# Kernel tuning notes

Measured on AMD Instinct MI355X. Metric: run time of the kernel, lower is better.

Reference implementation:

```python
import jax, jax.numpy as jnp
import numpy as np

DIM = 1024
N_HEAD = 16
N_KV_HEAD = 4
HEAD_DIM = DIM // N_HEAD  # 64
INTER = 2688
B, N = 2, 2048
EPS = 1e-6


def setup_inputs() -> dict:
    key = jax.random.key(0)
    ks = jax.random.split(key, 10)
    std = 0.02
    x = jax.random.normal(ks[0], (B, N, DIM), dtype=jnp.float32)
    # rotary embedding: theta = pos * 10000^(-2i/d), cos/sin of shape [N, HEAD_DIM//2]
    inv_freq = 1.0 / (10000.0 ** (np.arange(0, HEAD_DIM, 2, dtype=np.float32) / HEAD_DIM))
    t = np.arange(N, dtype=np.float32)
    ang = np.outer(t, inv_freq)  # [N, HEAD_DIM//2]
    rope_cos = jnp.asarray(np.cos(ang))
    rope_sin = jnp.asarray(np.sin(ang))
    mask = jnp.tril(jnp.ones((N, N), dtype=bool))  # True = attend
    return {
        "x": x,
        "w_attn_norm": jnp.ones((DIM,), jnp.float32),
        "w_ffn_norm": jnp.ones((DIM,), jnp.float32),
        "Wq": jax.random.normal(ks[1], (DIM, N_HEAD * HEAD_DIM), jnp.float32) * std,
        "Wkv": jax.random.normal(ks[2], (DIM, 2 * N_KV_HEAD * HEAD_DIM), jnp.float32) * std,
        "Wo": jax.random.normal(ks[3], (N_HEAD * HEAD_DIM, DIM), jnp.float32) * std,
        "W1": jax.random.normal(ks[4], (DIM, INTER), jnp.float32) * std,
        "W2": jax.random.normal(ks[5], (INTER, DIM), jnp.float32) * std,
        "W3": jax.random.normal(ks[6], (DIM, INTER), jnp.float32) * std,
        "rope_cos": rope_cos,
        "rope_sin": rope_sin,
        "mask": mask,
    }


def _rms_norm(x, w):
    # nn.functional.rms_norm: x / sqrt(mean(x^2) + eps) * w
    return x * jax.lax.rsqrt(jnp.mean(x * x, axis=-1, keepdims=True) + EPS) * w


def _apply_rope(x, cos, sin):
    # x: [b, n, h, d]; consecutive pairs (x[2k], x[2k+1]) form complex numbers
    xr = x[..., 0::2]
    xi = x[..., 1::2]
    c = cos[None, :, None, :]
    s = sin[None, :, None, :]
    yr = xr * c - xi * s
    yi = xr * s + xi * c
    return jnp.stack([yr, yi], axis=-1).reshape(x.shape)


def _block(x, w_attn_norm, w_ffn_norm, Wq, Wkv, Wo, W1, W2, W3, rope_cos, rope_sin, mask):
    b, n, _ = x.shape
    # --- attention (GQA, use_cache=False prefill) ---
    h = _rms_norm(x, w_attn_norm)
    q = (h @ Wq).reshape(b, n, N_HEAD, HEAD_DIM)
    kv = h @ Wkv
    k, v = jnp.split(kv, 2, axis=-1)
    k = k.reshape(b, n, N_KV_HEAD, HEAD_DIM)
    v = v.reshape(b, n, N_KV_HEAD, HEAD_DIM)
    q = _apply_rope(q, rope_cos, rope_sin)
    k = _apply_rope(k, rope_cos, rope_sin)
    # einops repeat 'b n h d -> b n (r h) d' == tile along head axis
    r = N_HEAD // N_KV_HEAD
    k = jnp.tile(k, (1, 1, r, 1))
    v = jnp.tile(v, (1, 1, r, 1))
    scale = HEAD_DIM ** -0.5
    scores = jnp.einsum('bnhd,bmhd->bhnm', q, k) * scale
    scores = jnp.where(mask[None, None, :, :], scores, jnp.finfo(scores.dtype).min)
    attn = jax.nn.softmax(scores, axis=-1)
    o = jnp.einsum('bhnm,bmhd->bnhd', attn, v).reshape(b, n, N_HEAD * HEAD_DIM)
    x = x + o @ Wo
    # --- SwiGLU MLP ---
    h2 = _rms_norm(x, w_ffn_norm)
    ff = (jax.nn.silu(h2 @ W1) * (h2 @ W3)) @ W2
    return x + ff


def reference(x, w_attn_norm, w_ffn_norm, Wq, Wkv, Wo, W1, W2, W3, rope_cos, rope_sin, mask):
    return _block(x, w_attn_norm, w_ffn_norm, Wq, Wkv, Wo, W1, W2, W3, rope_cos, rope_sin, mask)
```

## Files before the change

### kernel.cpp

```cpp
#include <hip/hip_runtime.h>

#define DIM 1024
#define NH 16
#define NKV 4
#define HD 64
#define INTER 2688
#define BB 2
#define NN 2048
#define MM (BB*NN)

typedef __attribute__((ext_vector_type(4))) float f32x4;
typedef __attribute__((ext_vector_type(16))) float f32x16;
typedef __attribute__((ext_vector_type(8))) short short8;

#define CROW(r,h) ((((r)&3)) + 8*((r)>>2) + 4*(h))

__device__ __forceinline__ unsigned short f2bf(float f) {
  union { float f; unsigned u; } v; v.f = f;
  unsigned r = v.u + 0x7fffu + ((v.u >> 16) & 1u);
  return (unsigned short)(r >> 16);
}

__device__ __forceinline__ void glds16(const unsigned short* g, unsigned short* l) {
  __builtin_amdgcn_global_load_lds(
      (const __attribute__((address_space(1))) void*)g,
      (__attribute__((address_space(3))) void*)l, 16, 0, 0);
}

__device__ __forceinline__ void xcd_map(int& bx, int& by) {
  int gx = gridDim.x;
  int nwg = gx * gridDim.y;
  int bid = (int)blockIdx.y * gx + (int)blockIdx.x;
  int cpx = nwg >> 3;
  int lg = (bid & 7) * cpx + (bid >> 3);
  bx = lg % gx;
  by = lg / gx;
}

__global__ void transpose_all(const float* __restrict__ Wq, const float* __restrict__ Wkv,
                              const float* __restrict__ Wo, const float* __restrict__ W1,
                              const float* __restrict__ W3, const float* __restrict__ W2,
                              unsigned short* __restrict__ WqkvT, unsigned short* __restrict__ WoT,
                              unsigned short* __restrict__ W1T, unsigned short* __restrict__ W3T,
                              unsigned short* __restrict__ W2T) {
  int tb = blockIdx.x;
  const float* src; unsigned short* dst; int K, Nc, t0;
  if (tb < 1024)        { src = Wq;  dst = WqkvT;                         K = 1024; Nc = 1024; t0 = tb; }
  else if (tb < 1536)   { src = Wkv; dst = WqkvT + (size_t)1024 * 1024;   K = 1024; Nc = 512;  t0 = tb - 1024; }
  else if (tb < 2560)   { src = Wo;  dst = WoT;                           K = 1024; Nc = 1024; t0 = tb - 1536; }
  else if (tb < 5248)   { src = W1;  dst = W1T;                           K = 1024; Nc = 2688; t0 = tb - 2560; }
  else if (tb < 7936)   { src = W3;  dst = W3T;                           K = 1024; Nc = 2688; t0 = tb - 5248; }
  else                  { src = W2;  dst = W2T;                           K = 2688; Nc = 1024; t0 = tb - 7936; }
  int ntx = Nc >> 5;
  int n0 = (t0 % ntx) * 32, k0 = (t0 / ntx) * 32;
  __shared__ float tile[32][33];
  int tx = threadIdx.x & 31, ty = threadIdx.x >> 5;
#pragma unroll
  for (int i = 0; i < 32; i += 8)
    tile[ty + i][tx] = src[(size_t)(k0 + ty + i) * Nc + n0 + tx];
  __syncthreads();
#pragma unroll
  for (int i = 0; i < 32; i += 8)
    dst[(size_t)(n0 + ty + i) * K + k0 + tx] = f2bf(tile[tx][ty + i]);
}

__global__ void rmsnorm_k(const float* __restrict__ x, const float* __restrict__ w,
                          unsigned short* __restrict__ h) {
  int row = blockIdx.x;
  int t = threadIdx.x;
  const float4* xr = (const float4*)(x + (size_t)row * DIM);
  float4 v = xr[t];
  float ss = v.x * v.x + v.y * v.y + v.z * v.z + v.w * v.w;
#pragma unroll
  for (int o = 1; o < 64; o <<= 1) ss += __shfl_xor(ss, o);
  __shared__ float ps[4];
  if ((t & 63) == 0) ps[t >> 6] = ss;
  __syncthreads();
  float r = rsqrtf((ps[0] + ps[1] + ps[2] + ps[3]) * (1.0f / DIM) + 1e-6f);
  const float4* wr = (const float4*)w;
  float4 wv = wr[t];
  ushort4 o4;
  o4.x = f2bf(v.x * r * wv.x);
  o4.y = f2bf(v.y * r * wv.y);
  o4.z = f2bf(v.z * r * wv.z);
  o4.w = f2bf(v.w * r * wv.w);
  *(ushort4*)(h + (size_t)row * DIM + t * 4) = o4;
}

template <bool RES>
__global__ __launch_bounds__(256, 3) void gemm_f32(
    const unsigned short* __restrict__ A, const unsigned short* __restrict__ Bt,
    const float* __restrict__ res, float* __restrict__ C, int Nc, int K) {
  __shared__ __align__(16) unsigned short Asm[3][128 * 32];
  __shared__ __align__(16) unsigned short Bsm[3][128 * 32];
  int tid = threadIdx.x;
  int w = tid >> 6, l = tid & 63;
  int bx, by;
  xcd_map(bx, by);
  int bm = by * 128, bn = bx * 128;
  int wr = (w >> 1) * 64, wc = (w & 1) * 64;
  int c0 = l & 15, g = l >> 4;

  int sr = w * 32 + (l >> 2);
  int sc = ((l & 3) ^ ((sr >> 1) & 3)) * 8;
  const unsigned short* gA0 = A + (size_t)(bm + sr) * K + sc;
  const unsigned short* gA1 = A + (size_t)(bm + sr + 16) * K + sc;
  const unsigned short* gB0 = Bt + (size_t)(bn + sr) * K + sc;
  const unsigned short* gB1 = Bt + (size_t)(bn + sr + 16) * K + sc;
  int ls0 = (w * 32) * 32, ls1 = (w * 32 + 16) * 32;

  int aoff[4], boff[4];
#pragma unroll
  for (int m = 0; m < 4; m++) {
    int ra = wr + m * 16 + c0;
    aoff[m] = ra * 32 + (g ^ ((ra >> 1) & 3)) * 8;
    int rb = wc + m * 16 + c0;
    boff[m] = rb * 32 + (g ^ ((rb >> 1) & 3)) * 8;
  }

  f32x4 acc[4][4] = {};
  int T = K / 32;
  glds16(gA0, &Asm[0][ls0]);
  glds16(gA1, &Asm[0][ls1]);
  glds16(gB0, &Bsm[0][ls0]);
  glds16(gB1, &Bsm[0][ls1]);
  glds16(gA0 + 32, &Asm[1][ls0]);
  glds16(gA1 + 32, &Asm[1][ls1]);
  glds16(gB0 + 32, &Bsm[1][ls0]);
  glds16(gB1 + 32, &Bsm[1][ls1]);
  int cur = 0;
  for (int t = 0; t < T; ++t) {
    if (t + 2 < T) {
      int nx = cur + 2; if (nx >= 3) nx -= 3;
      int ko = (t + 2) * 32;
      glds16(gA0 + ko, &Asm[nx][ls0]);
      glds16(gA1 + ko, &Asm[nx][ls1]);
      glds16(gB0 + ko, &Bsm[nx][ls0]);
      glds16(gB1 + ko, &Bsm[nx][ls1]);
      asm volatile("s_waitcnt vmcnt(8)" ::: "memory");
    } else if (t + 2 == T) {
      asm volatile("s_waitcnt vmcnt(4)" ::: "memory");
    } else {
      asm volatile("s_waitcnt vmcnt(0)" ::: "memory");
    }
    __builtin_amdgcn_s_barrier();
    __builtin_amdgcn_sched_barrier(0);
    const unsigned short* As = Asm[cur];
    const unsigned short* Bs = Bsm[cur];
    short8 af[4], bf[4];
#pragma unroll
    for (int m = 0; m < 4; m++) af[m] = *(const short8*)&As[aoff[m]];
#pragma unroll
    for (int n = 0; n < 4; n++) bf[n] = *(const short8*)&Bs[boff[n]];
    __builtin_amdgcn_s_setprio(1);
#pragma unroll
    for (int m = 0; m < 4; m++)
#pragma unroll
      for (int n = 0; n < 4; n++)
        acc[m][n] = __builtin_amdgcn_mfma_f32_16x16x32_bf16(af[m], bf[n], acc[m][n], 0, 0, 0);
    __builtin_amdgcn_s_setprio(0);
    asm volatile("s_waitcnt lgkmcnt(0)" ::: "memory");
    __builtin_amdgcn_sched_barrier(0);
    __builtin_amdgcn_s_barrier();
    cur = cur + 1 == 3 ? 0 : cur + 1;
  }
  int gq = l >> 4;
#pragma unroll
  for (int m = 0; m < 4; m++) {
#pragma unroll
    for (int i = 0; i < 4; i++) {
      int row = bm + wr + m * 16 + gq * 4 + i;
#pragma unroll
      for (int n = 0; n < 4; n++) {
        int col = bn + wc + n * 16 + c0;
        float v = acc[m][n][i];
        if (RES) v += res[(size_t)row * Nc + col];
        C[(size_t)row * Nc + col] = v;
      }
    }
  }
}

__global__ __launch_bounds__(256, 2) void gemm_ffn13(
    const unsigned short* __restrict__ A, const unsigned short* __restrict__ B1t,
    const unsigned short* __restrict__ B3t, unsigned short* __restrict__ G,
    int Nc, int K) {
  __shared__ __align__(16) unsigned short Asm[2][128 * 32];
  __shared__ __align__(16) unsigned short B1sm[2][128 * 32];
  __shared__ __align__(16) unsigned short B3sm[2][128 * 32];
  int tid = threadIdx.x;
  int w = tid >> 6, l = tid & 63;
  int bx, by;
  xcd_map(bx, by);
  int bm = by * 128, bn = bx * 128;
  int wr = (w >> 1) * 64, wc = (w & 1) * 64;
  int c0 = l & 15, g = l >> 4;

  int sr = w * 32 + (l >> 2);
  int sc = ((l & 3) ^ ((sr >> 1) & 3)) * 8;
  const unsigned short* gA0 = A + (size_t)(bm + sr) * K + sc;
  const unsigned short* gA1 = A + (size_t)(bm + sr + 16) * K + sc;
  const unsigned short* gB1a = B1t + (size_t)(bn + sr) * K + sc;
  const unsigned short* gB1b = B1t + (size_t)(bn + sr + 16) * K + sc;
  const unsigned short* gB3a = B3t + (size_t)(bn + sr) * K + sc;
  const unsigned short* gB3b = B3t + (size_t)(bn + sr + 16) * K + sc;
  int ls0 = (w * 32) * 32, ls1 = (w * 32 + 16) * 32;

  int aoff[4], boff[4];
#pragma unroll
  for (int m = 0; m < 4; m++) {
    int ra = wr + m * 16 + c0;
    aoff[m] = ra * 32 + (g ^ ((ra >> 1) & 3)) * 8;
    int rb = wc + m * 16 + c0;
    boff[m] = rb * 32 + (g ^ ((rb >> 1) & 3)) * 8;
  }

  f32x4 a1[4][4] = {};
  f32x4 a3[4][4] = {};
  int T = K / 32;
  glds16(gA0, &Asm[0][ls0]);
  glds16(gA1, &Asm[0][ls1]);
  glds16(gB1a, &B1sm[0][ls0]);
  glds16(gB1b, &B1sm[0][ls1]);
  glds16(gB3a, &B3sm[0][ls0]);
  glds16(gB3b, &B3sm[0][ls1]);
  __syncthreads();
  int buf = 0;
  for (int t = 0; t < T; ++t) {
    int nb = buf ^ 1;
    if (t + 1 < T) {
      int ko = (t + 1) * 32;
      glds16(gA0 + ko, &Asm[nb][ls0]);
      glds16(gA1 + ko, &Asm[nb][ls1]);
      glds16(gB1a + ko, &B1sm[nb][ls0]);
      glds16(gB1b + ko, &B1sm[nb][ls1]);
      glds16(gB3a + ko, &B3sm[nb][ls0]);
      glds16(gB3b + ko, &B3sm[nb][ls1]);
    }
    const unsigned short* As = Asm[buf];
    const unsigned short* B1s = B1sm[buf];
    const unsigned short* B3s = B3sm[buf];
    short8 af[4], b1f[4], b3f[4];
#pragma unroll
    for (int m = 0; m < 4; m++) af[m] = *(const short8*)&As[aoff[m]];
#pragma unroll
    for (int n = 0; n < 4; n++) {
      b1f[n] = *(const short8*)&B1s[boff[n]];
      b3f[n] = *(const short8*)&B3s[boff[n]];
    }
    __builtin_amdgcn_s_setprio(1);
#pragma unroll
    for (int m = 0; m < 4; m++)
#pragma unroll
      for (int n = 0; n < 4; n++) {
        a1[m][n] = __builtin_amdgcn_mfma_f32_16x16x32_bf16(af[m], b1f[n], a1[m][n], 0, 0, 0);
        a3[m][n] = __builtin_amdgcn_mfma_f32_16x16x32_bf16(af[m], b3f[n], a3[m][n], 0, 0, 0);
      }
    __builtin_amdgcn_s_setprio(0);
    __syncthreads();
    buf = nb;
  }
  int gq = l >> 4;
#pragma unroll
  for (int m = 0; m < 4; m++) {
#pragma unroll
    for (int i = 0; i < 4; i++) {
      int row = bm + wr + m * 16 + gq * 4 + i;
#pragma unroll
      for (int n = 0; n < 4; n++) {
        int col = bn + wc + n * 16 + c0;
        float x1 = a1[m][n][i], x3 = a3[m][n][i];
        float sg = x1 / (1.0f + __expf(-x1));
        G[(size_t)row * Nc + col] = f2bf(sg * x3);
      }
    }
  }
}

__global__ void prep_qkv(const float* __restrict__ qkv, const float* __restrict__ cosb,
                         const float* __restrict__ sinb, unsigned short* __restrict__ qb,
                         unsigned short* __restrict__ kb, unsigned short* __restrict__ vtb) {
  const float QS = 0.125f * 1.44269504f;
  int n = blockIdx.x, b = blockIdx.y;
  int t = threadIdx.x;
  const float* row = qkv + ((size_t)b * NN + n) * 1536;
#pragma unroll
  for (int p = t; p < 512; p += 256) {
    int head = p >> 5, j = p & 31;
    float xr = row[head * 64 + 2 * j], xi = row[head * 64 + 2 * j + 1];
    float c = cosb[n * 32 + j], s = sinb[n * 32 + j];
    size_t o = (((size_t)(b * NH + head)) * NN + n) * 64 + 2 * j;
    qb[o] = f2bf((xr * c - xi * s) * QS);
    qb[o + 1] = f2bf((xr * s + xi * c) * QS);
  }
  if (t < 128) {
    int kvh = t >> 5, j = t & 31;
    float xr = row[1024 + kvh * 64 + 2 * j], xi = row[1024 + kvh * 64 + 2 * j + 1];
    float c = cosb[n * 32 + j], s = sinb[n * 32 + j];
    size_t o = (((size_t)(b * NKV + kvh)) * NN + n) * 64 + 2 * j;
    kb[o] = f2bf(xr * c - xi * s);
    kb[o + 1] = f2bf(xr * s + xi * c);
  }
  {
    int kvh = t >> 6, d = t & 63;
    float v = row[1280 + kvh * 64 + d];
    vtb[(((size_t)(b * NKV + kvh)) * 64 + d) * NN + n] = f2bf(v);
  }
}

__global__ __launch_bounds__(256, 3) void attn_k(
    const unsigned short* __restrict__ qg_, const unsigned short* __restrict__ kg_,
    const unsigned short* __restrict__ vg_, unsigned short* __restrict__ ob) {
  __shared__ __align__(16) unsigned short Ksm[2][64 * 64];
  __shared__ __align__(16) unsigned short Vsm[2][64 * 64];
  int qb = (blockIdx.z == 0) ? (int)blockIdx.x : ((int)gridDim.x - 1 - (int)blockIdx.x);
  int h = blockIdx.y, b = blockIdx.z;
  int kvh = h & 3;
  int tid = threadIdx.x, w = tid >> 6, l = tid & 63;
  int q5 = l & 31, hi = l >> 5;
  int qwbase = qb * 128 + w * 32;
  int qgl = qwbase + q5;

  const unsigned short* Kg = kg_ + ((size_t)(b * NKV + kvh)) * NN * 64;
  const unsigned short* Vg = vg_ + ((size_t)(b * NKV + kvh)) * 64 * NN;

  short8 qf[4];
  {
    const unsigned short* qrow = qg_ + (((size_t)(b * NH + h)) * NN + qgl) * 64 + hi * 8;
#pragma unroll
    for (int d = 0; d < 4; d++) qf[d] = *(const short8*)(qrow + d * 16);
  }

  int srow = l >> 3;
  int schunk = (l & 7) ^ (srow & 7);
  const unsigned short* gK = Kg + (size_t)(w * 16 + srow) * 64 + schunk * 8;
  const unsigned short* gV = Vg + (size_t)(w * 16 + srow) * NN + schunk * 8;

  int nkt = qb * 2 + 2;
  int nkt_w = ((qwbase + 31) >> 6) + 1;

  f32x16 O0 = {}, O1 = {};
  float m_r = -1e30f, l_r = 0.0f;

  glds16(gK, &Ksm[0][w * 1024]);
  glds16(gK + 8 * 64, &Ksm[0][w * 1024 + 512]);
  glds16(gV, &Vsm[0][w * 1024]);
  glds16(gV + 8 * NN, &Vsm[0][w * 1024 + 512]);
  __syncthreads();

  int buf = 0;
  for (int kt = 0; kt < nkt; ++kt) {
    int n0 = kt * 64;
    if (kt + 1 < nkt) {
      int nb = buf ^ 1;
      glds16(gK + (size_t)(n0 + 64) * 64, &Ksm[nb][w * 1024]);
      glds16(gK + (size_t)(n0 + 64) * 64 + 8 * 64, &Ksm[nb][w * 1024 + 512]);
      glds16(gV + n0 + 64, &Vsm[nb][w * 1024]);
      glds16(gV + 8 * NN + n0 + 64, &Vsm[nb][w * 1024 + 512]);
    }
    if (kt < nkt_w) {
      const unsigned short* Ks = Ksm[buf];
      const unsigned short* Vs = Vsm[buf];
      f32x16 S[2];
      __builtin_amdgcn_s_setprio(1);
#pragma unroll
      for (int s = 0; s < 2; s++) {
        f32x16 acc = {};
        int row = s * 32 + q5;
#pragma unroll
        for (int d = 0; d < 4; d++) {
          int ch = (2 * d + hi) ^ (row & 7);
          short8 kf = *(const short8*)&Ks[row * 64 + ch * 8];
          acc = __builtin_amdgcn_mfma_f32_32x32x16_bf16(kf, qf[d], acc, 0, 0, 0);
        }
        S[s] = acc;
      }
      __builtin_amdgcn_s_setprio(0);
      if (kt == nkt_w - 1) {
#pragma unroll
        for (int s = 0; s < 2; s++)
#pragma unroll
          for (int r = 0; r < 16; r++) {
            int kg = n0 + s * 32 + CROW(r, hi);
            S[s][r] = (kg > qgl) ? -1e30f : S[s][r];
          }
      }
      float t16[16];
#pragma unroll
      for (int r = 0; r < 16; r++) t16[r] = fmaxf(S[0][r], S[1][r]);
#pragma unroll
      for (int k = 8; k >= 1; k >>= 1)
#pragma unroll
        for (int r = 0; r < k; r++) t16[r] = fmaxf(t16[r], t16[r + k]);
      float pm = fmaxf(t16[0], __shfl_xor(t16[0], 32));
      if (!__all(pm <= m_r + 8.0f)) {
        float mn = fmaxf(m_r, pm);
        float alpha = exp2f(m_r - mn);
        m_r = mn;
        l_r *= alpha;
        float ab[16];
#pragma unroll
        for (int r = 0; r < 16; r++) ab[r] = __shfl(alpha, CROW(r, 0) + 4 * hi);
#pragma unroll
        for (int r = 0; r < 16; r++) { O0[r] *= ab[r]; O1[r] *= ab[r]; }
      }
#pragma unroll
      for (int s = 0; s < 2; s++)
#pragma unroll
        for (int r = 0; r < 16; r++) S[s][r] = exp2f(S[s][r] - m_r);
      float u[16];
#pragma unroll
      for (int r = 0; r < 16; r++) u[r] = S[0][r] + S[1][r];
#pragma unroll
      for (int k = 8; k >= 1; k >>= 1)
#pragma unroll
        for (int r = 0; r < k; r++) u[r] += u[r + k];
      l_r += (u[0] + __shfl_xor(u[0], 32));
      short8 paf[4];
#pragma unroll
      for (int ks = 0; ks < 4; ks++) {
        const int s = ks >> 1, e = ks & 1;
        unsigned a0, a1, b0, b1;
        asm("v_cvt_pk_bf16_f32 %0, %1, %2" : "=v"(a0) : "v"(S[s][8*e+0]), "v"(S[s][8*e+1]));
        asm("v_cvt_pk_bf16_f32 %0, %1, %2" : "=v"(a1) : "v"(S[s][8*e+2]), "v"(S[s][8*e+3]));
        asm("v_cvt_pk_bf16_f32 %0, %1, %2" : "=v"(b0) : "v"(S[s][8*e+4]), "v"(S[s][8*e+5]));
        asm("v_cvt_pk_bf16_f32 %0, %1, %2" : "=v"(b1) : "v"(S[s][8*e+6]), "v"(S[s][8*e+7]));
        asm("v_permlane32_swap_b32 %0, %1" : "+v"(a0), "+v"(b0));
        asm("v_permlane32_swap_b32 %0, %1" : "+v"(a1), "+v"(b1));
        union { unsigned u4[4]; short8 s8; } pk;
        pk.u4[0] = a0; pk.u4[1] = a1; pk.u4[2] = b0; pk.u4[3] = b1;
        paf[ks] = pk.s8;
      }
      __builtin_amdgcn_s_setprio(1);
#pragma unroll
      for (int ks = 0; ks < 4; ks++) {
        int row0 = q5, row1 = 32 + q5;
        short8 vf0 = *(const short8*)&Vs[row0 * 64 + (((2 * ks + hi) ^ (row0 & 7)) * 8)];
        short8 vf1 = *(const short8*)&Vs[row1 * 64 + (((2 * ks + hi) ^ (row1 & 7)) * 8)];
        O0 = __builtin_amdgcn_mfma_f32_32x32x16_bf16(paf[ks], vf0, O0, 0, 0, 0);
        O1 = __builtin_amdgcn_mfma_f32_32x32x16_bf16(paf[ks], vf1, O1, 0, 0, 0);
      }
      __builtin_amdgcn_s_setprio(0);
    }
    __syncthreads();
    buf ^= 1;
  }
  float linv = 1.0f / l_r;
  float lb[16];
#pragma unroll
  for (int r = 0; r < 16; r++) lb[r] = __shfl(linv, CROW(r, 0) + 4 * hi);
#pragma unroll
  for (int r = 0; r < 16; r++) {
    int orow = qwbase + CROW(r, hi);
    size_t base = ((size_t)b * NN + orow) * 1024 + h * 64 + q5;
    ob[base] = f2bf(O0[r] * lb[r]);
    ob[base + 32] = f2bf(O1[r] * lb[r]);
  }
}

extern "C" void kernel_launch(void* const* d_in, const int* in_sizes, int n_in,
                              void* d_out, int out_size, void* d_ws, size_t ws_size,
                              hipStream_t stream) {
  (void)in_sizes; (void)n_in; (void)out_size; (void)ws_size;
  const float* x    = (const float*)d_in[0];
  const float* w_an = (const float*)d_in[1];
  const float* w_fn = (const float*)d_in[2];
  const float* Wq   = (const float*)d_in[3];
  const float* Wkv  = (const float*)d_in[4];
  const float* Wo   = (const float*)d_in[5];
  const float* W1   = (const float*)d_in[6];
  const float* W2   = (const float*)d_in[7];
  const float* W3   = (const float*)d_in[8];
  const float* cosb = (const float*)d_in[9];
  const float* sinb = (const float*)d_in[10];
  float* out = (float*)d_out;

  char* ws = (char*)d_ws;
  size_t off = 0;
  auto take = [&](size_t bytes) {
    size_t r = off;
    off += (bytes + 255) & ~(size_t)255;
    return r;
  };
  unsigned short* WqkvT = (unsigned short*)(ws + take((size_t)1536 * 1024 * 2));
  unsigned short* WoT   = (unsigned short*)(ws + take((size_t)1024 * 1024 * 2));
  unsigned short* W1T   = (unsigned short*)(ws + take((size_t)2688 * 1024 * 2));
  unsigned short* W3T   = (unsigned short*)(ws + take((size_t)2688 * 1024 * 2));
  unsigned short* W2T   = (unsigned short*)(ws + take((size_t)2688 * 1024 * 2));
  unsigned short* hA    = (unsigned short*)(ws + take((size_t)MM * DIM * 2));
  char* qkv_region = ws + take((size_t)MM * 1536 * 4);
  float* qkv = (float*)qkv_region;
  unsigned short* gbuf = (unsigned short*)qkv_region;
  unsigned short* qbuf = (unsigned short*)(ws + take((size_t)MM * DIM * 2));
  unsigned short* kbuf = (unsigned short*)(ws + take((size_t)BB * NKV * NN * HD * 2));
  unsigned short* vtb  = (unsigned short*)(ws + take((size_t)BB * NKV * NN * HD * 2));
  unsigned short* obuf = (unsigned short*)(ws + take((size_t)MM * DIM * 2));
  float* x2 = (float*)(ws + take((size_t)MM * DIM * 4));

  transpose_all<<<10624, 256, 0, stream>>>(Wq, Wkv, Wo, W1, W3, W2,
                                           WqkvT, WoT, W1T, W3T, W2T);
  rmsnorm_k<<<MM, 256, 0, stream>>>(x, w_an, hA);
  gemm_f32<false><<<dim3(1536 / 128, MM / 128), 256, 0, stream>>>(hA, WqkvT, nullptr, qkv, 1536, 1024);
  prep_qkv<<<dim3(NN, BB), 256, 0, stream>>>(qkv, cosb, sinb, qbuf, kbuf, vtb);
  attn_k<<<dim3(NN / 128, NH, BB), 256, 0, stream>>>(qbuf, kbuf, vtb, obuf);
  gemm_f32<true><<<dim3(1024 / 128, MM / 128), 256, 0, stream>>>(obuf, WoT, x, x2, 1024, 1024);
  rmsnorm_k<<<MM, 256, 0, stream>>>(x2, w_fn, hA);
  gemm_ffn13<<<dim3(INTER / 128, MM / 128), 256, 0, stream>>>(hA, W1T, W3T, gbuf, INTER, 1024);
  gemm_f32<true><<<dim3(1024 / 128, MM / 128), 256, 0, stream>>>(gbuf, W2T, x2, out, 1024, 2688);
}
```

Measured before the change: 269.1 us.

## Fuse RoPE and QKV layout into QKV GEMM epilogue; retile FFN13 GEMM

```diff
diff --git a/kernel.cpp b/kernel.cpp
--- a/kernel.cpp
+++ b/kernel.cpp
@@ -181,13 +181,15 @@
   }
 }
 
-__global__ __launch_bounds__(256, 2) void gemm_ffn13(
-    const unsigned short* __restrict__ A, const unsigned short* __restrict__ B1t,
-    const unsigned short* __restrict__ B3t, unsigned short* __restrict__ G,
-    int Nc, int K) {
-  __shared__ __align__(16) unsigned short Asm[2][128 * 32];
-  __shared__ __align__(16) unsigned short B1sm[2][128 * 32];
-  __shared__ __align__(16) unsigned short B3sm[2][128 * 32];
+__global__ __launch_bounds__(256, 3) void gemm_qkv(
+    const unsigned short* __restrict__ A, const unsigned short* __restrict__ Bt,
+    const float* __restrict__ cosb, const float* __restrict__ sinb,
+    unsigned short* __restrict__ qb, unsigned short* __restrict__ kb,
+    unsigned short* __restrict__ vtb) {
+  const int Nc = 1536, K = 1024;
+  const float QS = 0.125f * 1.44269504f;
+  __shared__ __align__(16) unsigned short Asm[3][128 * 32];
+  __shared__ __align__(16) unsigned short Bsm[3][128 * 32];
   int tid = threadIdx.x;
   int w = tid >> 6, l = tid & 63;
   int bx, by;
@@ -200,10 +202,8 @@
   int sc = ((l & 3) ^ ((sr >> 1) & 3)) * 8;
   const unsigned short* gA0 = A + (size_t)(bm + sr) * K + sc;
   const unsigned short* gA1 = A + (size_t)(bm + sr + 16) * K + sc;
-  const unsigned short* gB1a = B1t + (size_t)(bn + sr) * K + sc;
-  const unsigned short* gB1b = B1t + (size_t)(bn + sr + 16) * K + sc;
-  const unsigned short* gB3a = B3t + (size_t)(bn + sr) * K + sc;
-  const unsigned short* gB3b = B3t + (size_t)(bn + sr + 16) * K + sc;
+  const unsigned short* gB0 = Bt + (size_t)(bn + sr) * K + sc;
+  const unsigned short* gB1 = Bt + (size_t)(bn + sr + 16) * K + sc;
   int ls0 = (w * 32) * 32, ls1 = (w * 32 + 16) * 32;
 
   int aoff[4], boff[4];
@@ -215,36 +215,149 @@
     boff[m] = rb * 32 + (g ^ ((rb >> 1) & 3)) * 8;
   }
 
-  f32x4 a1[4][4] = {};
-  f32x4 a3[4][4] = {};
+  f32x4 acc[4][4] = {};
   int T = K / 32;
   glds16(gA0, &Asm[0][ls0]);
   glds16(gA1, &Asm[0][ls1]);
-  glds16(gB1a, &B1sm[0][ls0]);
-  glds16(gB1b, &B1sm[0][ls1]);
-  glds16(gB3a, &B3sm[0][ls0]);
-  glds16(gB3b, &B3sm[0][ls1]);
+  glds16(gB0, &Bsm[0][ls0]);
+  glds16(gB1, &Bsm[0][ls1]);
+  glds16(gA0 + 32, &Asm[1][ls0]);
+  glds16(gA1 + 32, &Asm[1][ls1]);
+  glds16(gB0 + 32, &Bsm[1][ls0]);
+  glds16(gB1 + 32, &Bsm[1][ls1]);
+  int cur = 0;
+  for (int t = 0; t < T; ++t) {
+    if (t + 2 < T) {
+      int nx = cur + 2; if (nx >= 3) nx -= 3;
+      int ko = (t + 2) * 32;
+      glds16(gA0 + ko, &Asm[nx][ls0]);
+      glds16(gA1 + ko, &Asm[nx][ls1]);
+      glds16(gB0 + ko, &Bsm[nx][ls0]);
+      glds16(gB1 + ko, &Bsm[nx][ls1]);
+      asm volatile("s_waitcnt vmcnt(8)" ::: "memory");
+    } else if (t + 2 == T) {
+      asm volatile("s_waitcnt vmcnt(4)" ::: "memory");
+    } else {
+      asm volatile("s_waitcnt vmcnt(0)" ::: "memory");
+    }
+    __builtin_amdgcn_s_barrier();
+    __builtin_amdgcn_sched_barrier(0);
+    const unsigned short* As = Asm[cur];
+    const unsigned short* Bs = Bsm[cur];
+    short8 af[4], bf[4];
+#pragma unroll
+    for (int m = 0; m < 4; m++) af[m] = *(const short8*)&As[aoff[m]];
+#pragma unroll
+    for (int n = 0; n < 4; n++) bf[n] = *(const short8*)&Bs[boff[n]];
+    __builtin_amdgcn_s_setprio(1);
+#pragma unroll
+    for (int m = 0; m < 4; m++)
+#pragma unroll
+      for (int n = 0; n < 4; n++)
+        acc[m][n] = __builtin_amdgcn_mfma_f32_16x16x32_bf16(af[m], bf[n], acc[m][n], 0, 0, 0);
+    __builtin_amdgcn_s_setprio(0);
+    asm volatile("s_waitcnt lgkmcnt(0)" ::: "memory");
+    __builtin_amdgcn_sched_barrier(0);
+    __builtin_amdgcn_s_barrier();
+    cur = cur + 1 == 3 ? 0 : cur + 1;
+  }
+  int gq = l >> 4;
+  int lodd = c0 & 1;
+#pragma unroll
+  for (int m = 0; m < 4; m++) {
+#pragma unroll
+    for (int i = 0; i < 4; i++) {
+      int row = bm + wr + m * 16 + gq * 4 + i;
+      int b = row >> 11, tok = row & (NN - 1);
+#pragma unroll
+      for (int n = 0; n < 4; n++) {
+        int col = bn + wc + n * 16 + c0;
+        float val = acc[m][n][i];
+        float partner = __shfl_xor(val, 1);
+        if (bn < 1024) {
+          int head = col >> 6, d = col & 63, j = d >> 1;
+          float c = cosb[tok * 32 + j], s = sinb[tok * 32 + j];
+          float r = lodd ? (partner * s + val * c) : (val * c - partner * s);
+          qb[(((size_t)(b * NH + head)) * NN + tok) * 64 + d] = f2bf(r * QS);
+        } else if (bn < 1280) {
+          int cc = col - 1024;
+          int kvh = cc >> 6, d = cc & 63, j = d >> 1;
+          float c = cosb[tok * 32 + j], s = sinb[tok * 32 + j];
+          float r = lodd ? (partner * s + val * c) : (val * c - partner * s);
+          kb[(((size_t)(b * NKV + kvh)) * NN + tok) * 64 + d] = f2bf(r);
+        } else {
+          int cc = col - 1280;
+          int kvh = cc >> 6, d = cc & 63;
+          vtb[(((size_t)(b * NKV + kvh)) * 64 + d) * NN + tok] = f2bf(val);
+        }
+      }
+    }
+  }
+}
+
+__global__ __launch_bounds__(256, 3) void gemm_ffn13(
+    const unsigned short* __restrict__ A, const unsigned short* __restrict__ B1t,
+    const unsigned short* __restrict__ B3t, unsigned short* __restrict__ G,
+    int Nc, int K) {
+  __shared__ __align__(16) unsigned short Asm[2 * 128 * 32];
+  __shared__ __align__(16) unsigned short B1sm[2 * 64 * 32];
+  __shared__ __align__(16) unsigned short B3sm[2 * 64 * 32];
+  int tid = threadIdx.x;
+  int w = tid >> 6, l = tid & 63;
+  int bx, by;
+  xcd_map(bx, by);
+  int bm = by * 128, bn = bx * 64;
+  int wr = (w >> 1) * 64, wc = (w & 1) * 32;
+  int c0 = l & 15, g = l >> 4;
+
+  int sr = w * 32 + (l >> 2);
+  int sb = w * 16 + (l >> 2);
+  int sc  = ((l & 3) ^ ((sr >> 1) & 3)) * 8;
+  int scb = ((l & 3) ^ ((sb >> 1) & 3)) * 8;
+  const unsigned short* gA0 = A + (size_t)(bm + sr) * K + sc;
+  const unsigned short* gA1 = A + (size_t)(bm + sr + 16) * K + sc;
+  const unsigned short* gB1 = B1t + (size_t)(bn + sb) * K + scb;
+  const unsigned short* gB3 = B3t + (size_t)(bn + sb) * K + scb;
+  int ls0 = (w * 32) * 32, ls1 = (w * 32 + 16) * 32, lsb = (w * 16) * 32;
+
+  int aoff[4], boff[2];
+#pragma unroll
+  for (int m = 0; m < 4; m++) {
+    int ra = wr + m * 16 + c0;
+    aoff[m] = ra * 32 + (g ^ ((ra >> 1) & 3)) * 8;
+  }
+#pragma unroll
+  for (int n = 0; n < 2; n++) {
+    int rb = wc + n * 16 + c0;
+    boff[n] = rb * 32 + (g ^ ((rb >> 1) & 3)) * 8;
+  }
+
+  f32x4 a1[4][2] = {};
+  f32x4 a3[4][2] = {};
+  int nsteps = K / 32;
+  glds16(gA0, &Asm[ls0]);
+  glds16(gA1, &Asm[ls1]);
+  glds16(gB1, &B1sm[lsb]);
+  glds16(gB3, &B3sm[lsb]);
   __syncthreads();
   int buf = 0;
-  for (int t = 0; t < T; ++t) {
+  for (int s = 0; s < nsteps; ++s) {
     int nb = buf ^ 1;
-    if (t + 1 < T) {
-      int ko = (t + 1) * 32;
-      glds16(gA0 + ko, &Asm[nb][ls0]);
-      glds16(gA1 + ko, &Asm[nb][ls1]);
-      glds16(gB1a + ko, &B1sm[nb][ls0]);
-      glds16(gB1b + ko, &B1sm[nb][ls1]);
-      glds16(gB3a + ko, &B3sm[nb][ls0]);
-      glds16(gB3b + ko, &B3sm[nb][ls1]);
-    }
-    const unsigned short* As = Asm[buf];
-    const unsigned short* B1s = B1sm[buf];
-    const unsigned short* B3s = B3sm[buf];
-    short8 af[4], b1f[4], b3f[4];
+    if (s + 1 < nsteps) {
+      int ko = (s + 1) * 32;
+      glds16(gA0 + ko, &Asm[nb * 4096 + ls0]);
+      glds16(gA1 + ko, &Asm[nb * 4096 + ls1]);
+      glds16(gB1 + ko, &B1sm[nb * 2048 + lsb]);
+      glds16(gB3 + ko, &B3sm[nb * 2048 + lsb]);
+    }
+    const unsigned short* As = &Asm[buf * 4096];
+    const unsigned short* B1s = &B1sm[buf * 2048];
+    const unsigned short* B3s = &B3sm[buf * 2048];
+    short8 af[4], b1f[2], b3f[2];
 #pragma unroll
     for (int m = 0; m < 4; m++) af[m] = *(const short8*)&As[aoff[m]];
 #pragma unroll
-    for (int n = 0; n < 4; n++) {
+    for (int n = 0; n < 2; n++) {
       b1f[n] = *(const short8*)&B1s[boff[n]];
       b3f[n] = *(const short8*)&B3s[boff[n]];
     }
@@ -252,7 +365,7 @@
 #pragma unroll
     for (int m = 0; m < 4; m++)
 #pragma unroll
-      for (int n = 0; n < 4; n++) {
+      for (int n = 0; n < 2; n++) {
         a1[m][n] = __builtin_amdgcn_mfma_f32_16x16x32_bf16(af[m], b1f[n], a1[m][n], 0, 0, 0);
         a3[m][n] = __builtin_amdgcn_mfma_f32_16x16x32_bf16(af[m], b3f[n], a3[m][n], 0, 0, 0);
       }
@@ -267,44 +380,13 @@
     for (int i = 0; i < 4; i++) {
       int row = bm + wr + m * 16 + gq * 4 + i;
 #pragma unroll
-      for (int n = 0; n < 4; n++) {
+      for (int n = 0; n < 2; n++) {
         int col = bn + wc + n * 16 + c0;
         float x1 = a1[m][n][i], x3 = a3[m][n][i];
         float sg = x1 / (1.0f + __expf(-x1));
         G[(size_t)row * Nc + col] = f2bf(sg * x3);
       }
     }
-  }
-}
-
-__global__ void prep_qkv(const float* __restrict__ qkv, const float* __restrict__ cosb,
-                         const float* __restrict__ sinb, unsigned short* __restrict__ qb,
-                         unsigned short* __restrict__ kb, unsigned short* __restrict__ vtb) {
-  const float QS = 0.125f * 1.44269504f;
-  int n = blockIdx.x, b = blockIdx.y;
-  int t = threadIdx.x;
-  const float* row = qkv + ((size_t)b * NN + n) * 1536;
-#pragma unroll
-  for (int p = t; p < 512; p += 256) {
-    int head = p >> 5, j = p & 31;
-    float xr = row[head * 64 + 2 * j], xi = row[head * 64 + 2 * j + 1];
-    float c = cosb[n * 32 + j], s = sinb[n * 32 + j];
-    size_t o = (((size_t)(b * NH + head)) * NN + n) * 64 + 2 * j;
-    qb[o] = f2bf((xr * c - xi * s) * QS);
-    qb[o + 1] = f2bf((xr * s + xi * c) * QS);
-  }
-  if (t < 128) {
-    int kvh = t >> 5, j = t & 31;
-    float xr = row[1024 + kvh * 64 + 2 * j], xi = row[1024 + kvh * 64 + 2 * j + 1];
-    float c = cosb[n * 32 + j], s = sinb[n * 32 + j];
-    size_t o = (((size_t)(b * NKV + kvh)) * NN + n) * 64 + 2 * j;
-    kb[o] = f2bf(xr * c - xi * s);
-    kb[o + 1] = f2bf(xr * s + xi * c);
-  }
-  {
-    int kvh = t >> 6, d = t & 63;
-    float v = row[1280 + kvh * 64 + d];
-    vtb[(((size_t)(b * NKV + kvh)) * 64 + d) * NN + n] = f2bf(v);
   }
 }
 
@@ -488,9 +570,7 @@
   unsigned short* W3T   = (unsigned short*)(ws + take((size_t)2688 * 1024 * 2));
   unsigned short* W2T   = (unsigned short*)(ws + take((size_t)2688 * 1024 * 2));
   unsigned short* hA    = (unsigned short*)(ws + take((size_t)MM * DIM * 2));
-  char* qkv_region = ws + take((size_t)MM * 1536 * 4);
-  float* qkv = (float*)qkv_region;
-  unsigned short* gbuf = (unsigned short*)qkv_region;
+  unsigned short* gbuf  = (unsigned short*)(ws + take((size_t)MM * INTER * 2));
   unsigned short* qbuf = (unsigned short*)(ws + take((size_t)MM * DIM * 2));
   unsigned short* kbuf = (unsigned short*)(ws + take((size_t)BB * NKV * NN * HD * 2));
   unsigned short* vtb  = (unsigned short*)(ws + take((size_t)BB * NKV * NN * HD * 2));
@@ -500,11 +580,11 @@
   transpose_all<<<10624, 256, 0, stream>>>(Wq, Wkv, Wo, W1, W3, W2,
                                            WqkvT, WoT, W1T, W3T, W2T);
   rmsnorm_k<<<MM, 256, 0, stream>>>(x, w_an, hA);
-  gemm_f32<false><<<dim3(1536 / 128, MM / 128), 256, 0, stream>>>(hA, WqkvT, nullptr, qkv, 1536, 1024);
-  prep_qkv<<<dim3(NN, BB), 256, 0, stream>>>(qkv, cosb, sinb, qbuf, kbuf, vtb);
+  gemm_qkv<<<dim3(1536 / 128, MM / 128), 256, 0, stream>>>(hA, WqkvT, cosb, sinb,
+                                                           qbuf, kbuf, vtb);
   attn_k<<<dim3(NN / 128, NH, BB), 256, 0, stream>>>(qbuf, kbuf, vtb, obuf);
   gemm_f32<true><<<dim3(1024 / 128, MM / 128), 256, 0, stream>>>(obuf, WoT, x, x2, 1024, 1024);
   rmsnorm_k<<<MM, 256, 0, stream>>>(x2, w_fn, hA);
-  gemm_ffn13<<<dim3(INTER / 128, MM / 128), 256, 0, stream>>>(hA, W1T, W3T, gbuf, INTER, 1024);
+  gemm_ffn13<<<dim3(INTER / 64, MM / 128), 256, 0, stream>>>(hA, W1T, W3T, gbuf, INTER, 1024);
   gemm_f32<true><<<dim3(1024 / 128, MM / 128), 256, 0, stream>>>(gbuf, W2T, x2, out, 1024, 2688);
 }
```

After: 260.3 us. 3.3% less time.
